# Kernel optimization log

Hardware: AMD Instinct MI355X
Metric: run time of the kernel (lower is better)

The kernel has to match this reference:

```python
import jax, jax.numpy as jnp
import numpy as np

TEMPERATURE = 0.5


def setup_inputs() -> dict:
    key = jax.random.key(0)
    k1, k2 = jax.random.split(key)
    emb_i = jax.random.normal(k1, (4096, 512), dtype=jnp.float32)
    emb_j = jax.random.normal(k2, (4096, 512), dtype=jnp.float32)
    return {"emb_i": emb_i, "emb_j": emb_j}


def reference(emb_i, emb_j):
    # NT-Xent (SimCLR) loss, vectorized over the original per-sample python loop.
    N = emb_i.shape[0]
    z_i = emb_i / jnp.linalg.norm(emb_i, axis=1, keepdims=True)
    z_j = emb_j / jnp.linalg.norm(emb_j, axis=1, keepdims=True)
    z = jnp.concatenate([z_i, z_j], axis=0)  # [2N, d]
    # cosine similarity of unit vectors == dot product
    sim = z @ z.T                             # [2N, 2N]
    exp_sim = jnp.exp(sim / TEMPERATURE)
    # denominator excludes self-similarity (the scatter-zero in the original)
    denom = exp_sim.sum(axis=1) - jnp.diagonal(exp_sim)
    idx = jnp.arange(2 * N)
    pos_idx = jnp.concatenate([jnp.arange(N) + N, jnp.arange(N)])
    num = exp_sim[idx, pos_idx]               # positive-pair similarities
    loss = -jnp.log(num / denom)
    return loss.mean()
```

## Files before the change

kernel.cpp:

```cpp
#include <hip/hip_runtime.h>
#include <hip/hip_bf16.h>

typedef __attribute__((ext_vector_type(4))) int i32x4;

#define AS1 __attribute__((address_space(1)))
#define AS3 __attribute__((address_space(3)))

#define DDIM 512
#define BK 64

__global__ __launch_bounds__(256) void norm_pd_kernel(
    const float* __restrict__ ei, const float* __restrict__ ej,
    unsigned char* __restrict__ zq, float* __restrict__ pd,
    float* __restrict__ rowsum, float* __restrict__ out, int N) {
  const int k = blockIdx.x;
  const int t = threadIdx.x;
  const float2 a = *reinterpret_cast<const float2*>(ei + (size_t)k * DDIM + t * 2);
  const float2 b = *reinterpret_cast<const float2*>(ej + (size_t)k * DDIM + t * 2);
  float sii = a.x * a.x + a.y * a.y;
  float sjj = b.x * b.x + b.y * b.y;
  float sij = a.x * b.x + a.y * b.y;
#pragma unroll
  for (int off = 32; off; off >>= 1) {
    sii += __shfl_down(sii, off);
    sjj += __shfl_down(sjj, off);
    sij += __shfl_down(sij, off);
  }
  __shared__ float red[3][4];
  if ((t & 63) == 0) { red[0][t >> 6] = sii; red[1][t >> 6] = sjj; red[2][t >> 6] = sij; }
  __syncthreads();
  sii = red[0][0] + red[0][1] + red[0][2] + red[0][3];
  sjj = red[1][0] + red[1][1] + red[1][2] + red[1][3];
  sij = red[2][0] + red[2][1] + red[2][2] + red[2][3];
  const float rsi = rsqrtf(sii), rsj = rsqrtf(sjj);

  const int qa0 = (int)rintf(127.0f * a.x * rsi);
  const int qa1 = (int)rintf(127.0f * a.y * rsi);
  const int qb0 = (int)rintf(127.0f * b.x * rsj);
  const int qb1 = (int)rintf(127.0f * b.y * rsj);
  const unsigned short wa = (unsigned short)(qa0 & 0xff) | ((unsigned short)(qa1 & 0xff) << 8);
  const unsigned short wb = (unsigned short)(qb0 & 0xff) | ((unsigned short)(qb1 & 0xff) << 8);
  *reinterpret_cast<unsigned short*>(zq + (size_t)k * DDIM + t * 2) = wa;
  *reinterpret_cast<unsigned short*>(zq + (size_t)(N + k) * DDIM + t * 2) = wb;
  if (t == 0) {
    pd[k] = sij * rsi * rsj;
    rowsum[k] = 0.0f;
    rowsum[N + k] = 0.0f;
    if (k == 0) out[0] = 0.0f;
  }
}


#define MFMAI8(A, B, C) __builtin_amdgcn_mfma_i32_16x16x64_i8((A), (B), (C), 0, 0, 0)

__global__ __launch_bounds__(256, 4) void simloss_main(
    const unsigned char* __restrict__ zq, float* __restrict__ rowsum, int nwg) {
  const int orig = blockIdx.x;
  const int q = nwg >> 3, r8 = nwg & 7;
  const int xcd = orig & 7, pos0 = orig >> 3;
  const int t0 = (xcd < r8 ? xcd * (q + 1) : r8 * (q + 1) + (xcd - r8) * q) + pos0;

  const float ff = sqrtf(8.0f * (float)t0 + 1.0f);
  int by = (int)((ff - 1.0f) * 0.5f);
  while ((by + 1) * (by + 2) / 2 <= t0) ++by;
  while (by * (by + 1) / 2 > t0) --by;
  const int bx = t0 - by * (by + 1) / 2;

  const int row0 = bx * 128;
  const int col0 = by * 128;

  __shared__ unsigned char lds[2][2][8192];

  const int tid = threadIdx.x;
  const int w = tid >> 6;
  const int l = tid & 63;
  const int wr = (w >> 1) * 64;
  const int wc = (w & 1) * 64;
  const int lrow = l & 15;
  const int g = l >> 4;

  i32x4 acc[4][4] = {};

  auto stage_half = [&](int buf, int half, int baserow, int k0) {
#pragma unroll
    for (int it = 0; it < 2; ++it) {
      const int p = it * 256 + tid;
      const int row = p >> 2;
      const int s = p & 3;
      const int gs = (s - (row >> 1)) & 3;
      const unsigned char* src = zq + (size_t)(baserow + row) * DDIM + k0 + gs * 16;
      char* dst = (char*)&lds[buf][half][0] + (unsigned)((it * 256 + w * 64) * 16);
      __builtin_amdgcn_global_load_lds((const AS1 void*)src, (AS3 void*)dst, 16, 0, 0);
    }
  };

  auto compute = [&](int buf) {
    const unsigned char* ab = &lds[buf][0][0];
    const unsigned char* bb = &lds[buf][1][0];
    i32x4 Af[4], Bf[4];
#pragma unroll
    for (int mf = 0; mf < 4; ++mf) {
      const int r = wr + mf * 16 + lrow;
      Af[mf] = *reinterpret_cast<const i32x4*>(ab + r * 64 + (((g + (r >> 1)) & 3) << 4));
    }
#pragma unroll
    for (int nf = 0; nf < 4; ++nf) {
      const int c = wc + nf * 16 + lrow;
      Bf[nf] = *reinterpret_cast<const i32x4*>(bb + c * 64 + (((g + (c >> 1)) & 3) << 4));
    }
#pragma unroll
    for (int mf = 0; mf < 4; ++mf)
#pragma unroll
      for (int nf = 0; nf < 4; ++nf)
        acc[mf][nf] = MFMAI8(Af[mf], Bf[nf], acc[mf][nf]);
  };

  stage_half(0, 0, row0, 0);
  stage_half(0, 1, col0, 0);

#pragma unroll
  for (int t = 0; t < 7; ++t) {
    const int buf = t & 1;
    stage_half(buf ^ 1, 0, row0, (t + 1) * BK);
    stage_half(buf ^ 1, 1, col0, (t + 1) * BK);
    asm volatile("s_waitcnt vmcnt(4)" ::: "memory");
    __builtin_amdgcn_s_barrier();
    compute(buf);
    __builtin_amdgcn_s_barrier();
  }
  asm volatile("s_waitcnt vmcnt(0)" ::: "memory");
  __builtin_amdgcn_s_barrier();
  compute(1);

  const float SC = 2.0f * 1.44269504088896340736f / 16129.0f;
  const int lgrp = l >> 4;
  const int lcol = l & 15;

  float e[4][4][4];
#pragma unroll
  for (int mf = 0; mf < 4; ++mf)
#pragma unroll
    for (int nf = 0; nf < 4; ++nf)
#pragma unroll
      for (int rg = 0; rg < 4; ++rg)
        e[mf][nf][rg] = exp2f((float)acc[mf][nf][rg] * SC);

#pragma unroll
  for (int mf = 0; mf < 4; ++mf) {
    float rs[4];
#pragma unroll
    for (int rg = 0; rg < 4; ++rg) {
      float s = 0.0f;
#pragma unroll
      for (int nf = 0; nf < 4; ++nf) s += e[mf][nf][rg];
      rs[rg] = s;
    }
#pragma unroll
    for (int off = 1; off < 16; off <<= 1) {
#pragma unroll
      for (int rg = 0; rg < 4; ++rg) rs[rg] += __shfl_xor(rs[rg], off);
    }
    if (lcol == 0) {
      const int rowb = row0 + wr + mf * 16 + lgrp * 4;
#pragma unroll
      for (int rg = 0; rg < 4; ++rg) atomicAdd(&rowsum[rowb + rg], rs[rg]);
    }
  }

  if (bx != by) {
#pragma unroll
    for (int nf = 0; nf < 4; ++nf) {
      float cs = 0.0f;
#pragma unroll
      for (int mf = 0; mf < 4; ++mf)
#pragma unroll
        for (int rg = 0; rg < 4; ++rg) cs += e[mf][nf][rg];
      cs += __shfl_xor(cs, 16);
      cs += __shfl_xor(cs, 32);
      if (lgrp == 0) atomicAdd(&rowsum[col0 + wc + nf * 16 + lcol], cs);
    }
  }
}

__global__ __launch_bounds__(1024) void finalize_kernel(
    const float* __restrict__ rowsum, const float* __restrict__ pd,
    float* __restrict__ out, int M, int N) {
  const int i = blockIdx.x * 1024 + threadIdx.x;
  const float E2 = 7.38905609893065f;
  float acc = 0.0f;
  if (i < M) {
    const float denom = rowsum[i] - E2;
    const int kk = (i < N) ? i : (i - N);
    acc = logf(denom) - 2.0f * pd[kk];
  }
#pragma unroll
  for (int off = 32; off; off >>= 1) acc += __shfl_down(acc, off);
  __shared__ float red[16];
  const int t = threadIdx.x;
  if ((t & 63) == 0) red[t >> 6] = acc;
  __syncthreads();
  if (t < 64) {
    float s = (t < 16) ? red[t] : 0.0f;
#pragma unroll
    for (int off = 8; off; off >>= 1) s += __shfl_down(s, off);
    if (t == 0) atomicAdd(out, s / (float)M);
  }
}

extern "C" void kernel_launch(void* const* d_in, const int* in_sizes, int n_in,
                              void* d_out, int out_size, void* d_ws, size_t ws_size,
                              hipStream_t stream) {
  const float* ei = (const float*)d_in[0];
  const float* ej = (const float*)d_in[1];
  float* out = (float*)d_out;

  const int N = in_sizes[0] / DDIM;
  const int M = 2 * N;
  const int NT = M / 128;
  const int NTRI = NT * (NT + 1) / 2;

  char* ws = (char*)d_ws;
  unsigned char* zq = (unsigned char*)ws;
  float* pd = (float*)(ws + (size_t)M * DDIM);
  float* rowsum = (float*)(ws + (size_t)M * DDIM + (size_t)N * 4);

  norm_pd_kernel<<<N, 256, 0, stream>>>(ei, ej, zq, pd, rowsum, out, N);
  simloss_main<<<NTRI, 256, 0, stream>>>(zq, rowsum, NTRI);
  finalize_kernel<<<(M + 1023) / 1024, 1024, 0, stream>>>(rowsum, pd, out, M, N);
}
```

Measured before the change: 46.05 us.

## Quantize embeddings to FP4 and use scaled f8f6f4 MFMA for similarity

The normalized embeddings are now encoded as FP4 (E2M1) values scaled by 32 and packed two per byte, replacing the int8 encoding. The similarity GEMM uses the 32x32x64 scaled f8f6f4 MFMA in FP4 mode with float accumulators, and the LDS layout, staging and epilogue reductions are reworked to match. This halves the global and LDS traffic and the number of K iterations, which targets load and compute cost in the main kernel. In exchange, FP4 precision with only 8 magnitude levels makes the similarities, and so the exp-based loss, much less accurate, which may break tolerance.

```diff
diff --git a/kernel.cpp b/kernel.cpp
--- a/kernel.cpp
+++ b/kernel.cpp
@@ -2,12 +2,24 @@
 #include <hip/hip_bf16.h>
 
 typedef __attribute__((ext_vector_type(4))) int i32x4;
+typedef __attribute__((ext_vector_type(8))) int i32x8;
+typedef __attribute__((ext_vector_type(16))) float f32x16;
 
 #define AS1 __attribute__((address_space(1)))
 #define AS3 __attribute__((address_space(3)))
 
 #define DDIM 512
-#define BK 64
+#define RB 256
+
+__device__ inline unsigned enc_fp4(float x) {
+  const unsigned s = (__float_as_uint(x) >> 31) << 3;
+  const float y = fabsf(x);
+  unsigned m;
+  if (y < 1.75f)      m = (unsigned)rintf(y * 2.0f);
+  else if (y < 3.5f)  m = 4u + (unsigned)rintf(y - 2.0f);
+  else                m = (y >= 5.0f) ? 7u : 6u;
+  return s | m;
+}
 
 __global__ __launch_bounds__(256) void norm_pd_kernel(
     const float* __restrict__ ei, const float* __restrict__ ej,
@@ -34,14 +46,12 @@
   sij = red[2][0] + red[2][1] + red[2][2] + red[2][3];
   const float rsi = rsqrtf(sii), rsj = rsqrtf(sjj);
 
-  const int qa0 = (int)rintf(127.0f * a.x * rsi);
-  const int qa1 = (int)rintf(127.0f * a.y * rsi);
-  const int qb0 = (int)rintf(127.0f * b.x * rsj);
-  const int qb1 = (int)rintf(127.0f * b.y * rsj);
-  const unsigned short wa = (unsigned short)(qa0 & 0xff) | ((unsigned short)(qa1 & 0xff) << 8);
-  const unsigned short wb = (unsigned short)(qb0 & 0xff) | ((unsigned short)(qb1 & 0xff) << 8);
-  *reinterpret_cast<unsigned short*>(zq + (size_t)k * DDIM + t * 2) = wa;
-  *reinterpret_cast<unsigned short*>(zq + (size_t)(N + k) * DDIM + t * 2) = wb;
+  const float sa0 = 32.0f * a.x * rsi, sa1 = 32.0f * a.y * rsi;
+  const float sb0 = 32.0f * b.x * rsj, sb1 = 32.0f * b.y * rsj;
+  const unsigned char ba = (unsigned char)(enc_fp4(sa0) | (enc_fp4(sa1) << 4));
+  const unsigned char bb = (unsigned char)(enc_fp4(sb0) | (enc_fp4(sb1) << 4));
+  zq[(size_t)k * RB + t] = ba;
+  zq[(size_t)(N + k) * RB + t] = bb;
   if (t == 0) {
     pd[k] = sij * rsi * rsj;
     rowsum[k] = 0.0f;
@@ -50,8 +60,6 @@
   }
 }
 
-
-#define MFMAI8(A, B, C) __builtin_amdgcn_mfma_i32_16x16x64_i8((A), (B), (C), 0, 0, 0)
 
 __global__ __launch_bounds__(256, 4) void simloss_main(
     const unsigned char* __restrict__ zq, float* __restrict__ rowsum, int nwg) {
@@ -69,115 +77,114 @@
   const int row0 = bx * 128;
   const int col0 = by * 128;
 
-  __shared__ unsigned char lds[2][2][8192];
+  __shared__ __align__(16) unsigned char lds[2][2][8192];
 
   const int tid = threadIdx.x;
   const int w = tid >> 6;
   const int l = tid & 63;
-  const int wr = (w >> 1) * 64;
-  const int wc = (w & 1) * 64;
-  const int lrow = l & 15;
-  const int g = l >> 4;
-
-  i32x4 acc[4][4] = {};
-
-  auto stage_half = [&](int buf, int half, int baserow, int k0) {
-#pragma unroll
-    for (int it = 0; it < 2; ++it) {
-      const int p = it * 256 + tid;
-      const int row = p >> 2;
-      const int s = p & 3;
-      const int gs = (s - (row >> 1)) & 3;
-      const unsigned char* src = zq + (size_t)(baserow + row) * DDIM + k0 + gs * 16;
-      char* dst = (char*)&lds[buf][half][0] + (unsigned)((it * 256 + w * 64) * 16);
-      __builtin_amdgcn_global_load_lds((const AS1 void*)src, (AS3 void*)dst, 16, 0, 0);
+  const int trw = (w >> 1) * 64;
+  const int tcw = (w & 1) * 64;
+  const int lh = l >> 5;
+  const int l31 = l & 31;
+
+  f32x16 acc[2][2] = {};
+
+  auto stage = [&](int buf, int t) {
+    const int kb = t * 64;
+#pragma unroll
+    for (int half = 0; half < 2; ++half) {
+      const int baserow = half ? col0 : row0;
+#pragma unroll
+      for (int it = 0; it < 2; ++it) {
+        const int idx = it * 256 + tid;
+        const int r = idx & 127;
+        const int c = idx >> 7;
+        const unsigned char* src = zq + (size_t)(baserow + r) * RB + kb + c * 16;
+        char* dst = (char*)&lds[buf][half][0] + (unsigned)((it * 256 + w * 64) * 16);
+        __builtin_amdgcn_global_load_lds((const AS1 void*)src, (AS3 void*)dst, 16, 0, 0);
+      }
     }
   };
 
   auto compute = [&](int buf) {
     const unsigned char* ab = &lds[buf][0][0];
     const unsigned char* bb = &lds[buf][1][0];
-    i32x4 Af[4], Bf[4];
-#pragma unroll
-    for (int mf = 0; mf < 4; ++mf) {
-      const int r = wr + mf * 16 + lrow;
-      Af[mf] = *reinterpret_cast<const i32x4*>(ab + r * 64 + (((g + (r >> 1)) & 3) << 4));
-    }
-#pragma unroll
-    for (int nf = 0; nf < 4; ++nf) {
-      const int c = wc + nf * 16 + lrow;
-      Bf[nf] = *reinterpret_cast<const i32x4*>(bb + c * 64 + (((g + (c >> 1)) & 3) << 4));
-    }
-#pragma unroll
-    for (int mf = 0; mf < 4; ++mf)
-#pragma unroll
-      for (int nf = 0; nf < 4; ++nf)
-        acc[mf][nf] = MFMAI8(Af[mf], Bf[nf], acc[mf][nf]);
+    i32x4 A4[2][2], B4[2][2];
+#pragma unroll
+    for (int mf = 0; mf < 2; ++mf)
+#pragma unroll
+      for (int kk = 0; kk < 2; ++kk) {
+        const int cch = kk * 2 + lh;
+        A4[mf][kk] = *reinterpret_cast<const i32x4*>(ab + cch * 2048 + (trw + mf * 32 + l31) * 16);
+        B4[mf][kk] = *reinterpret_cast<const i32x4*>(bb + cch * 2048 + (tcw + mf * 32 + l31) * 16);
+      }
+#pragma unroll
+    for (int mf = 0; mf < 2; ++mf)
+#pragma unroll
+      for (int nf = 0; nf < 2; ++nf)
+#pragma unroll
+        for (int kk = 0; kk < 2; ++kk) {
+          const i32x8 a8 = {A4[mf][kk].x, A4[mf][kk].y, A4[mf][kk].z, A4[mf][kk].w, 0, 0, 0, 0};
+          const i32x8 b8 = {B4[nf][kk].x, B4[nf][kk].y, B4[nf][kk].z, B4[nf][kk].w, 0, 0, 0, 0};
+          acc[mf][nf] = __builtin_amdgcn_mfma_scale_f32_32x32x64_f8f6f4(
+              a8, b8, acc[mf][nf], 4, 4,
+              0, 0x7f7f7f7f,
+              0, 0x7f7f7f7f);
+        }
   };
 
-  stage_half(0, 0, row0, 0);
-  stage_half(0, 1, col0, 0);
-
-#pragma unroll
-  for (int t = 0; t < 7; ++t) {
-    const int buf = t & 1;
-    stage_half(buf ^ 1, 0, row0, (t + 1) * BK);
-    stage_half(buf ^ 1, 1, col0, (t + 1) * BK);
+  stage(0, 0);
+#pragma unroll
+  for (int t = 0; t < 3; ++t) {
+    stage((t & 1) ^ 1, t + 1);
     asm volatile("s_waitcnt vmcnt(4)" ::: "memory");
     __builtin_amdgcn_s_barrier();
-    compute(buf);
+    compute(t & 1);
     __builtin_amdgcn_s_barrier();
   }
   asm volatile("s_waitcnt vmcnt(0)" ::: "memory");
   __builtin_amdgcn_s_barrier();
   compute(1);
 
-  const float SC = 2.0f * 1.44269504088896340736f / 16129.0f;
-  const int lgrp = l >> 4;
-  const int lcol = l & 15;
-
-  float e[4][4][4];
-#pragma unroll
-  for (int mf = 0; mf < 4; ++mf)
-#pragma unroll
-    for (int nf = 0; nf < 4; ++nf)
-#pragma unroll
-      for (int rg = 0; rg < 4; ++rg)
-        e[mf][nf][rg] = exp2f((float)acc[mf][nf][rg] * SC);
-
-#pragma unroll
-  for (int mf = 0; mf < 4; ++mf) {
-    float rs[4];
-#pragma unroll
-    for (int rg = 0; rg < 4; ++rg) {
-      float s = 0.0f;
-#pragma unroll
-      for (int nf = 0; nf < 4; ++nf) s += e[mf][nf][rg];
-      rs[rg] = s;
-    }
-#pragma unroll
-    for (int off = 1; off < 16; off <<= 1) {
-#pragma unroll
-      for (int rg = 0; rg < 4; ++rg) rs[rg] += __shfl_xor(rs[rg], off);
-    }
-    if (lcol == 0) {
-      const int rowb = row0 + wr + mf * 16 + lgrp * 4;
-#pragma unroll
-      for (int rg = 0; rg < 4; ++rg) atomicAdd(&rowsum[rowb + rg], rs[rg]);
+  const float SC = 2.0f * 1.44269504088896340736f / 1024.0f;
+
+#pragma unroll
+  for (int mf = 0; mf < 2; ++mf)
+#pragma unroll
+    for (int nf = 0; nf < 2; ++nf)
+#pragma unroll
+      for (int rg = 0; rg < 16; ++rg)
+        acc[mf][nf][rg] = exp2f(acc[mf][nf][rg] * SC);
+
+#pragma unroll
+  for (int mf = 0; mf < 2; ++mf) {
+    float rs[16];
+#pragma unroll
+    for (int rg = 0; rg < 16; ++rg) rs[rg] = acc[mf][0][rg] + acc[mf][1][rg];
+#pragma unroll
+    for (int off = 1; off < 32; off <<= 1) {
+#pragma unroll
+      for (int rg = 0; rg < 16; ++rg) rs[rg] += __shfl_xor(rs[rg], off);
+    }
+    if (l31 == 0) {
+#pragma unroll
+      for (int rg = 0; rg < 16; ++rg) {
+        const int row = row0 + trw + mf * 32 + (rg & 3) + 8 * (rg >> 2) + 4 * lh;
+        atomicAdd(&rowsum[row], rs[rg]);
+      }
     }
   }
 
   if (bx != by) {
 #pragma unroll
-    for (int nf = 0; nf < 4; ++nf) {
+    for (int nf = 0; nf < 2; ++nf) {
       float cs = 0.0f;
 #pragma unroll
-      for (int mf = 0; mf < 4; ++mf)
-#pragma unroll
-        for (int rg = 0; rg < 4; ++rg) cs += e[mf][nf][rg];
-      cs += __shfl_xor(cs, 16);
+      for (int mf = 0; mf < 2; ++mf)
+#pragma unroll
+        for (int rg = 0; rg < 16; ++rg) cs += acc[mf][nf][rg];
       cs += __shfl_xor(cs, 32);
-      if (lgrp == 0) atomicAdd(&rowsum[col0 + wc + nf * 16 + lcol], cs);
+      if (l < 32) atomicAdd(&rowsum[col0 + tcw + nf * 32 + l], cs);
     }
   }
 }
@@ -221,8 +228,8 @@
 
   char* ws = (char*)d_ws;
   unsigned char* zq = (unsigned char*)ws;
-  float* pd = (float*)(ws + (size_t)M * DDIM);
-  float* rowsum = (float*)(ws + (size_t)M * DDIM + (size_t)N * 4);
+  float* pd = (float*)(ws + (size_t)M * RB);
+  float* rowsum = (float*)(ws + (size_t)M * RB + (size_t)N * 4);
 
   norm_pd_kernel<<<N, 256, 0, stream>>>(ei, ej, zq, pd, rowsum, out, N);
   simloss_main<<<NTRI, 256, 0, stream>>>(zq, rowsum, NTRI);
```

After: 54.67 us. 18.7% more time.

## Make simloss kernel persistent with cross-tile prefetch of next tile

Applied to the files above, without the earlier changes.

Replaces the one-workgroup-per-triangle-tile launch with a fixed grid of 1024 persistent workgroups. Each workgroup walks a contiguous range of tiles within its XCD and prefetches the first K-slice of the next tile during the last MMA step of the current one. This removes launch and tail overhead and hides each tile's pipeline prologue. The risks are load imbalance, since each block gets 2-3 tiles, and the assumption that NTRI is divisible by 8, which silently drops the remainder tiles otherwise.

```diff
diff --git a/kernel.cpp b/kernel.cpp
--- a/kernel.cpp
+++ b/kernel.cpp
@@ -54,20 +54,17 @@
 #define MFMAI8(A, B, C) __builtin_amdgcn_mfma_i32_16x16x64_i8((A), (B), (C), 0, 0, 0)
 
 __global__ __launch_bounds__(256, 4) void simloss_main(
-    const unsigned char* __restrict__ zq, float* __restrict__ rowsum, int nwg) {
+    const unsigned char* __restrict__ zq, float* __restrict__ rowsum,
+    int ntri, int nblk) {
   const int orig = blockIdx.x;
-  const int q = nwg >> 3, r8 = nwg & 7;
-  const int xcd = orig & 7, pos0 = orig >> 3;
-  const int t0 = (xcd < r8 ? xcd * (q + 1) : r8 * (q + 1) + (xcd - r8) * q) + pos0;
-
-  const float ff = sqrtf(8.0f * (float)t0 + 1.0f);
-  int by = (int)((ff - 1.0f) * 0.5f);
-  while ((by + 1) * (by + 2) / 2 <= t0) ++by;
-  while (by * (by + 1) / 2 > t0) --by;
-  const int bx = t0 - by * (by + 1) / 2;
-
-  const int row0 = bx * 128;
-  const int col0 = by * 128;
+  const int xcd = orig & 7, p = orig >> 3;
+  const int per_xcd = ntri >> 3;
+  const int bpx = nblk >> 3;
+  const int q = per_xcd / bpx, r = per_xcd % bpx;
+  const int start = p * q + (p < r ? p : r);
+  const int cnt = q + (p < r ? 1 : 0);
+  const int tbeg = xcd * per_xcd + start;
+  const int tend = tbeg + cnt;
 
   __shared__ unsigned char lds[2][2][8192];
 
@@ -79,20 +76,32 @@
   const int lrow = l & 15;
   const int g = l >> 4;
 
+  auto decode = [&](int t, int& bx, int& by) {
+    const float ff = sqrtf(8.0f * (float)t + 1.0f);
+    by = (int)((ff - 1.0f) * 0.5f);
+    while ((by + 1) * (by + 2) / 2 <= t) ++by;
+    while (by * (by + 1) / 2 > t) --by;
+    bx = t - by * (by + 1) / 2;
+  };
+
+  auto stage = [&](int buf, int arow, int brow, int k0) {
+#pragma unroll
+    for (int half = 0; half < 2; ++half) {
+      const int baserow = half ? brow : arow;
+#pragma unroll
+      for (int it = 0; it < 2; ++it) {
+        const int pp = it * 256 + tid;
+        const int row = pp >> 2;
+        const int s = pp & 3;
+        const int gs = (s - (row >> 1)) & 3;
+        const unsigned char* src = zq + (size_t)(baserow + row) * DDIM + k0 + gs * 16;
+        char* dst = (char*)&lds[buf][half][0] + (unsigned)((it * 256 + w * 64) * 16);
+        __builtin_amdgcn_global_load_lds((const AS1 void*)src, (AS3 void*)dst, 16, 0, 0);
+      }
+    }
+  };
+
   i32x4 acc[4][4] = {};
-
-  auto stage_half = [&](int buf, int half, int baserow, int k0) {
-#pragma unroll
-    for (int it = 0; it < 2; ++it) {
-      const int p = it * 256 + tid;
-      const int row = p >> 2;
-      const int s = p & 3;
-      const int gs = (s - (row >> 1)) & 3;
-      const unsigned char* src = zq + (size_t)(baserow + row) * DDIM + k0 + gs * 16;
-      char* dst = (char*)&lds[buf][half][0] + (unsigned)((it * 256 + w * 64) * 16);
-      __builtin_amdgcn_global_load_lds((const AS1 void*)src, (AS3 void*)dst, 16, 0, 0);
-    }
-  };
 
   auto compute = [&](int buf) {
     const unsigned char* ab = &lds[buf][0][0];
@@ -100,13 +109,13 @@
     i32x4 Af[4], Bf[4];
 #pragma unroll
     for (int mf = 0; mf < 4; ++mf) {
-      const int r = wr + mf * 16 + lrow;
-      Af[mf] = *reinterpret_cast<const i32x4*>(ab + r * 64 + (((g + (r >> 1)) & 3) << 4));
+      const int rr = wr + mf * 16 + lrow;
+      Af[mf] = *reinterpret_cast<const i32x4*>(ab + rr * 64 + (((g + (rr >> 1)) & 3) << 4));
     }
 #pragma unroll
     for (int nf = 0; nf < 4; ++nf) {
-      const int c = wc + nf * 16 + lrow;
-      Bf[nf] = *reinterpret_cast<const i32x4*>(bb + c * 64 + (((g + (c >> 1)) & 3) << 4));
+      const int cc = wc + nf * 16 + lrow;
+      Bf[nf] = *reinterpret_cast<const i32x4*>(bb + cc * 64 + (((g + (cc >> 1)) & 3) << 4));
     }
 #pragma unroll
     for (int mf = 0; mf < 4; ++mf)
@@ -115,70 +124,94 @@
         acc[mf][nf] = MFMAI8(Af[mf], Bf[nf], acc[mf][nf]);
   };
 
-  stage_half(0, 0, row0, 0);
-  stage_half(0, 1, col0, 0);
-
-#pragma unroll
-  for (int t = 0; t < 7; ++t) {
-    const int buf = t & 1;
-    stage_half(buf ^ 1, 0, row0, (t + 1) * BK);
-    stage_half(buf ^ 1, 1, col0, (t + 1) * BK);
-    asm volatile("s_waitcnt vmcnt(4)" ::: "memory");
-    __builtin_amdgcn_s_barrier();
-    compute(buf);
-    __builtin_amdgcn_s_barrier();
-  }
-  asm volatile("s_waitcnt vmcnt(0)" ::: "memory");
-  __builtin_amdgcn_s_barrier();
-  compute(1);
-
   const float SC = 2.0f * 1.44269504088896340736f / 16129.0f;
   const int lgrp = l >> 4;
   const int lcol = l & 15;
 
-  float e[4][4][4];
-#pragma unroll
-  for (int mf = 0; mf < 4; ++mf)
-#pragma unroll
-    for (int nf = 0; nf < 4; ++nf)
-#pragma unroll
-      for (int rg = 0; rg < 4; ++rg)
-        e[mf][nf][rg] = exp2f((float)acc[mf][nf][rg] * SC);
-
-#pragma unroll
-  for (int mf = 0; mf < 4; ++mf) {
-    float rs[4];
-#pragma unroll
-    for (int rg = 0; rg < 4; ++rg) {
-      float s = 0.0f;
-#pragma unroll
-      for (int nf = 0; nf < 4; ++nf) s += e[mf][nf][rg];
-      rs[rg] = s;
-    }
-#pragma unroll
-    for (int off = 1; off < 16; off <<= 1) {
-#pragma unroll
-      for (int rg = 0; rg < 4; ++rg) rs[rg] += __shfl_xor(rs[rg], off);
-    }
-    if (lcol == 0) {
-      const int rowb = row0 + wr + mf * 16 + lgrp * 4;
-#pragma unroll
-      for (int rg = 0; rg < 4; ++rg) atomicAdd(&rowsum[rowb + rg], rs[rg]);
-    }
-  }
-
-  if (bx != by) {
-#pragma unroll
-    for (int nf = 0; nf < 4; ++nf) {
-      float cs = 0.0f;
-#pragma unroll
-      for (int mf = 0; mf < 4; ++mf)
-#pragma unroll
-        for (int rg = 0; rg < 4; ++rg) cs += e[mf][nf][rg];
-      cs += __shfl_xor(cs, 16);
-      cs += __shfl_xor(cs, 32);
-      if (lgrp == 0) atomicAdd(&rowsum[col0 + wc + nf * 16 + lcol], cs);
-    }
+  if (tbeg >= tend) return;
+
+  int bx, by;
+  decode(tbeg, bx, by);
+  int row0 = bx * 128, col0 = by * 128;
+  int nbx, nby, nrow0 = 0, ncol0 = 0;
+
+  stage(0, row0, col0, 0);
+  int buf = 0;
+
+  for (int ti = tbeg; ti < tend; ++ti) {
+    const bool havenext = (ti + 1 < tend);
+    if (havenext) {
+      decode(ti + 1, nbx, nby);
+      nrow0 = nbx * 128; ncol0 = nby * 128;
+    }
+#pragma unroll
+    for (int t = 0; t < 8; ++t) {
+      if (t < 7) {
+        stage(buf ^ 1, row0, col0, (t + 1) * BK);
+        asm volatile("s_waitcnt vmcnt(4)" ::: "memory");
+      } else if (havenext) {
+        stage(buf ^ 1, nrow0, ncol0, 0);
+        asm volatile("s_waitcnt vmcnt(4)" ::: "memory");
+      } else {
+        asm volatile("s_waitcnt vmcnt(0)" ::: "memory");
+      }
+      __builtin_amdgcn_s_barrier();
+      compute(buf);
+      __builtin_amdgcn_s_barrier();
+      buf ^= 1;
+    }
+
+    float e[4][4][4];
+#pragma unroll
+    for (int mf = 0; mf < 4; ++mf)
+#pragma unroll
+      for (int nf = 0; nf < 4; ++nf)
+#pragma unroll
+        for (int rg = 0; rg < 4; ++rg)
+          e[mf][nf][rg] = exp2f((float)acc[mf][nf][rg] * SC);
+
+#pragma unroll
+    for (int mf = 0; mf < 4; ++mf) {
+      float rs[4];
+#pragma unroll
+      for (int rg = 0; rg < 4; ++rg) {
+        float s = 0.0f;
+#pragma unroll
+        for (int nf = 0; nf < 4; ++nf) s += e[mf][nf][rg];
+        rs[rg] = s;
+      }
+#pragma unroll
+      for (int off = 1; off < 16; off <<= 1) {
+#pragma unroll
+        for (int rg = 0; rg < 4; ++rg) rs[rg] += __shfl_xor(rs[rg], off);
+      }
+      if (lcol == 0) {
+        const int rowb = row0 + wr + mf * 16 + lgrp * 4;
+#pragma unroll
+        for (int rg = 0; rg < 4; ++rg) atomicAdd(&rowsum[rowb + rg], rs[rg]);
+      }
+    }
+
+    if (bx != by) {
+#pragma unroll
+      for (int nf = 0; nf < 4; ++nf) {
+        float cs = 0.0f;
+#pragma unroll
+        for (int mf = 0; mf < 4; ++mf)
+#pragma unroll
+          for (int rg = 0; rg < 4; ++rg) cs += e[mf][nf][rg];
+        cs += __shfl_xor(cs, 16);
+        cs += __shfl_xor(cs, 32);
+        if (lgrp == 0) atomicAdd(&rowsum[col0 + wc + nf * 16 + lcol], cs);
+      }
+    }
+
+#pragma unroll
+    for (int mf = 0; mf < 4; ++mf)
+#pragma unroll
+      for (int nf = 0; nf < 4; ++nf)
+        acc[mf][nf] = i32x4{0, 0, 0, 0};
+    bx = nbx; by = nby; row0 = nrow0; col0 = ncol0;
   }
 }
 
@@ -218,6 +251,7 @@
   const int M = 2 * N;
   const int NT = M / 128;
   const int NTRI = NT * (NT + 1) / 2;
+  const int NBLK = 1024;
 
   char* ws = (char*)d_ws;
   unsigned char* zq = (unsigned char*)ws;
@@ -225,6 +259,6 @@
   float* rowsum = (float*)(ws + (size_t)M * DDIM + (size_t)N * 4);
 
   norm_pd_kernel<<<N, 256, 0, stream>>>(ei, ej, zq, pd, rowsum, out, N);
-  simloss_main<<<NTRI, 256, 0, stream>>>(zq, rowsum, NTRI);
+  simloss_main<<<NBLK, 256, 0, stream>>>(zq, rowsum, NTRI, NBLK);
   finalize_kernel<<<(M + 1023) / 1024, 1024, 0, stream>>>(rowsum, pd, out, M, N);
 }
```

After: 48.08 us. 4.4% more time.

## Triple-buffer int8 GEMM staging and fold finalize into last-block ticket

Applied to the files above, without the earlier changes.

The main similarity kernel moves from double to triple buffering of the LDS tiles, keeping two K-slices in flight, with waitcnt thresholds adjusted to match. The separate finalize kernel is removed: each workgroup takes a ticket atomically after its rowsum atomics, and the last one computes the log-loss reduction and writes the output. This removes one kernel launch and gives more latency hiding. In exchange, LDS use per block rises to 48KB, which may lower occupancy, and the single last block does the serial final reduction.

```diff
diff --git a/kernel.cpp b/kernel.cpp
--- a/kernel.cpp
+++ b/kernel.cpp
@@ -12,7 +12,8 @@
 __global__ __launch_bounds__(256) void norm_pd_kernel(
     const float* __restrict__ ei, const float* __restrict__ ej,
     unsigned char* __restrict__ zq, float* __restrict__ pd,
-    float* __restrict__ rowsum, float* __restrict__ out, int N) {
+    float* __restrict__ rowsum, float* __restrict__ out,
+    int* __restrict__ ticket, int N) {
   const int k = blockIdx.x;
   const int t = threadIdx.x;
   const float2 a = *reinterpret_cast<const float2*>(ei + (size_t)k * DDIM + t * 2);
@@ -46,7 +47,7 @@
     pd[k] = sij * rsi * rsj;
     rowsum[k] = 0.0f;
     rowsum[N + k] = 0.0f;
-    if (k == 0) out[0] = 0.0f;
+    if (k == 0) { out[0] = 0.0f; ticket[0] = 0; }
   }
 }
 
@@ -54,7 +55,9 @@
 #define MFMAI8(A, B, C) __builtin_amdgcn_mfma_i32_16x16x64_i8((A), (B), (C), 0, 0, 0)
 
 __global__ __launch_bounds__(256, 4) void simloss_main(
-    const unsigned char* __restrict__ zq, float* __restrict__ rowsum, int nwg) {
+    const unsigned char* __restrict__ zq, float* __restrict__ rowsum,
+    const float* __restrict__ pd, float* __restrict__ out,
+    int* __restrict__ ticket, int nwg, int M, int N) {
   const int orig = blockIdx.x;
   const int q = nwg >> 3, r8 = nwg & 7;
   const int xcd = orig & 7, pos0 = orig >> 3;
@@ -69,7 +72,7 @@
   const int row0 = bx * 128;
   const int col0 = by * 128;
 
-  __shared__ unsigned char lds[2][2][8192];
+  __shared__ unsigned char lds[3][2][8192];
 
   const int tid = threadIdx.x;
   const int w = tid >> 6;
@@ -81,16 +84,20 @@
 
   i32x4 acc[4][4] = {};
 
-  auto stage_half = [&](int buf, int half, int baserow, int k0) {
-#pragma unroll
-    for (int it = 0; it < 2; ++it) {
-      const int p = it * 256 + tid;
-      const int row = p >> 2;
-      const int s = p & 3;
-      const int gs = (s - (row >> 1)) & 3;
-      const unsigned char* src = zq + (size_t)(baserow + row) * DDIM + k0 + gs * 16;
-      char* dst = (char*)&lds[buf][half][0] + (unsigned)((it * 256 + w * 64) * 16);
-      __builtin_amdgcn_global_load_lds((const AS1 void*)src, (AS3 void*)dst, 16, 0, 0);
+  auto stage = [&](int buf, int k0) {
+#pragma unroll
+    for (int half = 0; half < 2; ++half) {
+      const int baserow = half ? col0 : row0;
+#pragma unroll
+      for (int it = 0; it < 2; ++it) {
+        const int pp = it * 256 + tid;
+        const int row = pp >> 2;
+        const int s = pp & 3;
+        const int gs = (s - (row >> 1)) & 3;
+        const unsigned char* src = zq + (size_t)(baserow + row) * DDIM + k0 + gs * 16;
+        char* dst = (char*)&lds[buf][half][0] + (unsigned)((it * 256 + w * 64) * 16);
+        __builtin_amdgcn_global_load_lds((const AS1 void*)src, (AS3 void*)dst, 16, 0, 0);
+      }
     }
   };
 
@@ -100,13 +107,13 @@
     i32x4 Af[4], Bf[4];
 #pragma unroll
     for (int mf = 0; mf < 4; ++mf) {
-      const int r = wr + mf * 16 + lrow;
-      Af[mf] = *reinterpret_cast<const i32x4*>(ab + r * 64 + (((g + (r >> 1)) & 3) << 4));
+      const int rr = wr + mf * 16 + lrow;
+      Af[mf] = *reinterpret_cast<const i32x4*>(ab + rr * 64 + (((g + (rr >> 1)) & 3) << 4));
     }
 #pragma unroll
     for (int nf = 0; nf < 4; ++nf) {
-      const int c = wc + nf * 16 + lrow;
-      Bf[nf] = *reinterpret_cast<const i32x4*>(bb + c * 64 + (((g + (c >> 1)) & 3) << 4));
+      const int cc = wc + nf * 16 + lrow;
+      Bf[nf] = *reinterpret_cast<const i32x4*>(bb + cc * 64 + (((g + (cc >> 1)) & 3) << 4));
     }
 #pragma unroll
     for (int mf = 0; mf < 4; ++mf)
@@ -115,24 +122,26 @@
         acc[mf][nf] = MFMAI8(Af[mf], Bf[nf], acc[mf][nf]);
   };
 
-  stage_half(0, 0, row0, 0);
-  stage_half(0, 1, col0, 0);
-
-#pragma unroll
-  for (int t = 0; t < 7; ++t) {
-    const int buf = t & 1;
-    stage_half(buf ^ 1, 0, row0, (t + 1) * BK);
-    stage_half(buf ^ 1, 1, col0, (t + 1) * BK);
-    asm volatile("s_waitcnt vmcnt(4)" ::: "memory");
+  stage(0, 0);
+  stage(1, BK);
+
+#pragma unroll
+  for (int t = 0; t < 8; ++t) {
+    if (t < 6) {
+      stage((t + 2) % 3, (t + 2) * BK);
+      asm volatile("s_waitcnt vmcnt(8)" ::: "memory");
+    } else if (t == 6) {
+      asm volatile("s_waitcnt vmcnt(4)" ::: "memory");
+    } else {
+      asm volatile("s_waitcnt vmcnt(0)" ::: "memory");
+    }
     __builtin_amdgcn_s_barrier();
-    compute(buf);
+    compute(t % 3);
     __builtin_amdgcn_s_barrier();
   }
-  asm volatile("s_waitcnt vmcnt(0)" ::: "memory");
-  __builtin_amdgcn_s_barrier();
-  compute(1);
 
   const float SC = 2.0f * 1.44269504088896340736f / 16129.0f;
+  const float E2 = 7.38905609893065f;
   const int lgrp = l >> 4;
   const int lcol = l & 15;
 
@@ -180,30 +189,24 @@
       if (lgrp == 0) atomicAdd(&rowsum[col0 + wc + nf * 16 + lcol], cs);
     }
   }
-}
-
-__global__ __launch_bounds__(1024) void finalize_kernel(
-    const float* __restrict__ rowsum, const float* __restrict__ pd,
-    float* __restrict__ out, int M, int N) {
-  const int i = blockIdx.x * 1024 + threadIdx.x;
-  const float E2 = 7.38905609893065f;
-  float acc = 0.0f;
-  if (i < M) {
-    const float denom = rowsum[i] - E2;
-    const int kk = (i < N) ? i : (i - N);
-    acc = logf(denom) - 2.0f * pd[kk];
-  }
-#pragma unroll
-  for (int off = 32; off; off >>= 1) acc += __shfl_down(acc, off);
-  __shared__ float red[16];
-  const int t = threadIdx.x;
-  if ((t & 63) == 0) red[t >> 6] = acc;
+
+  __threadfence();
+  __shared__ int is_last;
+  if (tid == 0) is_last = (atomicAdd(ticket, 1) == nwg - 1);
   __syncthreads();
-  if (t < 64) {
-    float s = (t < 16) ? red[t] : 0.0f;
-#pragma unroll
-    for (int off = 8; off; off >>= 1) s += __shfl_down(s, off);
-    if (t == 0) atomicAdd(out, s / (float)M);
+  if (is_last) {
+    float accv = 0.0f;
+    for (int i = tid; i < M; i += 256) {
+      const float denom = atomicAdd(&rowsum[i], 0.0f) - E2;
+      const int kk = (i < N) ? i : (i - N);
+      accv += logf(denom) - 2.0f * pd[kk];
+    }
+#pragma unroll
+    for (int off = 32; off; off >>= 1) accv += __shfl_down(accv, off);
+    __shared__ float fred[4];
+    if ((tid & 63) == 0) fred[tid >> 6] = accv;
+    __syncthreads();
+    if (tid == 0) out[0] = (fred[0] + fred[1] + fred[2] + fred[3]) / (float)M;
   }
 }
 
@@ -223,8 +226,8 @@
   unsigned char* zq = (unsigned char*)ws;
   float* pd = (float*)(ws + (size_t)M * DDIM);
   float* rowsum = (float*)(ws + (size_t)M * DDIM + (size_t)N * 4);
-
-  norm_pd_kernel<<<N, 256, 0, stream>>>(ei, ej, zq, pd, rowsum, out, N);
-  simloss_main<<<NTRI, 256, 0, stream>>>(zq, rowsum, NTRI);
-  finalize_kernel<<<(M + 1023) / 1024, 1024, 0, stream>>>(rowsum, pd, out, M, N);
+  int* ticket = (int*)(ws + (size_t)M * DDIM + (size_t)N * 4 + (size_t)M * 4);
+
+  norm_pd_kernel<<<N, 256, 0, stream>>>(ei, ej, zq, pd, rowsum, out, ticket, N);
+  simloss_main<<<NTRI, 256, 0, stream>>>(zq, rowsum, pd, out, ticket, NTRI, M, N);
 }
```

After: 165.4 us. 3.59x slower.
